# Kernel tuning notes

Measured on AMD Instinct MI355X. Metric: run time of the kernel, lower is better.

The kernel has to match this reference:

```python
import jax, jax.numpy as jnp
import numpy as np

N_NODES = 50000
N_EDGES = 800000
IN_CH = 128
HID = 32
HEADS = 4
OUT_CH = 16
NEG_SLOPE = 0.2  # PyG GATConv default LeakyReLU slope


def setup_inputs() -> dict:
    key = jax.random.key(0)
    ks = jax.random.split(key, 12)
    x = jax.random.normal(ks[0], (N_NODES, IN_CH), dtype=jnp.float32)
    edge_index = jax.random.randint(ks[1], (2, N_EDGES), 0, N_NODES, dtype=jnp.int32)
    edge_attr = jax.random.uniform(ks[2], (N_EDGES,), dtype=jnp.float32)
    s = 0.1
    W1 = jax.random.normal(ks[3], (IN_CH, HEADS * HID), dtype=jnp.float32) * s
    a_src1 = jax.random.normal(ks[4], (HEADS, HID), dtype=jnp.float32) * s
    a_dst1 = jax.random.normal(ks[5], (HEADS, HID), dtype=jnp.float32) * s
    b1 = jnp.zeros((HEADS * HID,), dtype=jnp.float32)
    W2 = jax.random.normal(ks[6], (HEADS * HID, OUT_CH), dtype=jnp.float32) * s
    a_src2 = jax.random.normal(ks[7], (1, OUT_CH), dtype=jnp.float32) * s
    a_dst2 = jax.random.normal(ks[8], (1, OUT_CH), dtype=jnp.float32) * s
    b2 = jnp.zeros((OUT_CH,), dtype=jnp.float32)
    return {"x": x, "edge_index": edge_index, "edge_attr": edge_attr,
            "W1": W1, "a_src1": a_src1, "a_dst1": a_dst1, "b1": b1,
            "W2": W2, "a_src2": a_src2, "a_dst2": a_dst2, "b2": b2}


def gat_conv(x, src, dst, num_nodes, W, a_src, a_dst, bias, concat):
    H, C = a_src.shape
    h = (x @ W).reshape(-1, H, C)              # [N,H,C]
    al_src = jnp.sum(h * a_src, axis=-1)       # [N,H]
    al_dst = jnp.sum(h * a_dst, axis=-1)       # [N,H]
    e = jax.nn.leaky_relu(al_src[src] + al_dst[dst], NEG_SLOPE)  # [E,H]
    # segment softmax over incoming edges of each destination node
    m = jax.ops.segment_max(e, dst, num_segments=num_nodes)
    ex = jnp.exp(e - m[dst])
    denom = jax.ops.segment_sum(ex, dst, num_segments=num_nodes)
    alpha = ex / (denom[dst] + 1e-16)          # [E,H]
    out = jax.ops.segment_sum(h[src] * alpha[..., None], dst, num_segments=num_nodes)  # [N,H,C]
    out = out.reshape(num_nodes, H * C) if concat else out.mean(axis=1)
    return out + bias


def reference(x, edge_index, edge_attr, W1, a_src1, a_dst1, b1, W2, a_src2, a_dst2, b2):
    # edge_attr is ignored by GATConv when edge_dim is None (PyG default)
    N = x.shape[0]
    loop = jnp.arange(N, dtype=edge_index.dtype)  # PyG add_self_loops=True
    src = jnp.concatenate([edge_index[0], loop])
    dst = jnp.concatenate([edge_index[1], loop])
    h = jax.nn.elu(gat_conv(x, src, dst, N, W1, a_src1, a_dst1, b1, True))
    out = gat_conv(h, src, dst, N, W2, a_src2, a_dst2, b2, False)
    return jax.nn.log_softmax(out, axis=1)
```

## Files before the change

### kernel.cpp

```cpp
#include <hip/hip_runtime.h>

#define N_NODESC 50000
#define E0C      800000
#define E_TOTC   850000
#define IN_CHC   128
#define HCC      128
#define HEADSC   4
#define OUT_CHC  16
#define NEG_SLOPE 0.2f
#define G1_ROWS  32
#define NBUCK    196
#define BNODES   256
#define SBLK     128
#define CHUNK    6656

__device__ __forceinline__ float lrelu(float v){ return v > 0.f ? v : NEG_SLOPE * v; }

__device__ __forceinline__ unsigned int f2bf(float f){
  unsigned int b = __float_as_uint(f);
  return (b + 0x7fffu + ((b >> 16) & 1u)) >> 16;
}
__device__ __forceinline__ float bf2f(unsigned int lo16){
  return __uint_as_float(lo16 << 16);
}
__device__ __forceinline__ int xswz(int r, int k){ return r ^ (((k >> 4) & 7) << 2); }

__global__ void __launch_bounds__(512) k_gemm1(const float* __restrict__ x, const float* __restrict__ W1,
        const float* __restrict__ a_s, const float* __restrict__ a_d,
        unsigned int* __restrict__ h1b, float* __restrict__ al_s, float* __restrict__ al_d)
{
  __shared__ __align__(16) float Wl[IN_CHC*HCC];
  __shared__ __align__(16) float xT[IN_CHC][G1_ROWS];
  int tid = threadIdx.x;
  for (int i = tid*4; i < IN_CHC*HCC; i += 512*4)
    *(float4*)&Wl[i] = *(const float4*)&W1[i];
  int row0 = blockIdx.x * G1_ROWS;
  {
    int r  = tid >> 4;
    int kc = (tid & 15) * 8;
    int rr = row0 + r; if (rr > N_NODESC-1) rr = N_NODESC-1;
    const float* xp = &x[(size_t)rr*IN_CHC + kc];
    int sc = xswz(r, kc);
    #pragma unroll
    for (int j = 0; j < 8; j += 4){
      float4 v = *(const float4*)&xp[j];
      xT[kc+j+0][sc] = v.x;
      xT[kc+j+1][sc] = v.y;
      xT[kc+j+2][sc] = v.z;
      xT[kc+j+3][sc] = v.w;
    }
  }
  __syncthreads();
  int wave = tid >> 6, lane = tid & 63;
  int c0 = lane * 2;
  int rbase = wave * 4;
  float acc[4][2];
  #pragma unroll
  for (int j = 0; j < 4; j++){ acc[j][0] = 0.f; acc[j][1] = 0.f; }
  #pragma unroll 4
  for (int k = 0; k < IN_CHC; k++){
    float2 w  = *(const float2*)&Wl[k*HCC + c0];
    float4 xa = *(const float4*)&xT[k][xswz(rbase, k)];
    acc[0][0] = fmaf(xa.x, w.x, acc[0][0]); acc[0][1] = fmaf(xa.x, w.y, acc[0][1]);
    acc[1][0] = fmaf(xa.y, w.x, acc[1][0]); acc[1][1] = fmaf(xa.y, w.y, acc[1][1]);
    acc[2][0] = fmaf(xa.z, w.x, acc[2][0]); acc[2][1] = fmaf(xa.z, w.y, acc[2][1]);
    acc[3][0] = fmaf(xa.w, w.x, acc[3][0]); acc[3][1] = fmaf(xa.w, w.y, acc[3][1]);
  }
  float as0 = a_s[c0], as1 = a_s[c0+1];
  float ad0 = a_d[c0], ad1 = a_d[c0+1];
  #pragma unroll
  for (int j = 0; j < 4; j++){
    int row = row0 + rbase + j;
    if (row >= N_NODESC) break;
    h1b[(size_t)row*64 + lane] = f2bf(acc[j][0]) | (f2bf(acc[j][1]) << 16);
    float ps = acc[j][0]*as0 + acc[j][1]*as1;
    float pd = acc[j][0]*ad0 + acc[j][1]*ad1;
    #pragma unroll
    for (int m = 1; m < 16; m <<= 1){ ps += __shfl_xor(ps, m, 64); pd += __shfl_xor(pd, m, 64); }
    if ((lane & 15) == 0){
      al_s[row*HEADSC + (lane>>4)] = ps;
      al_d[row*HEADSC + (lane>>4)] = pd;
    }
  }
}

__global__ void __launch_bounds__(256) k_binA(const int* __restrict__ ei, int* __restrict__ bh){
  __shared__ int h[NBUCK];
  int tid = threadIdx.x, b = blockIdx.x;
  for (int i = tid; i < NBUCK; i += 256) h[i] = 0;
  __syncthreads();
  int e0 = b*CHUNK, e1 = e0 + CHUNK; if (e1 > E_TOTC) e1 = E_TOTC;
  for (int e = e0 + tid; e < e1; e += 256){
    int d = (e < E0C) ? ei[E0C + e] : (e - E0C);
    atomicAdd(&h[d >> 8], 1);
  }
  __syncthreads();
  for (int i = tid; i < NBUCK; i += 256) bh[b*NBUCK + i] = h[i];
}

__global__ void __launch_bounds__(256) k_binscan(int* __restrict__ bh, int* __restrict__ bstart){
  __shared__ int buf[256];
  int tid = threadIdx.x;
  int tot = 0;
  if (tid < NBUCK)
    for (int b = 0; b < SBLK; b++) tot += bh[b*NBUCK + tid];
  buf[tid] = (tid < NBUCK) ? tot : 0;
  __syncthreads();
  #pragma unroll
  for (int off = 1; off < 256; off <<= 1){
    int t = (tid >= off) ? buf[tid - off] : 0;
    __syncthreads();
    buf[tid] += t; __syncthreads();
  }
  int excl = buf[tid] - ((tid < NBUCK) ? tot : 0);
  if (tid < NBUCK) bstart[tid] = excl;
  if (tid == 0) bstart[NBUCK] = E_TOTC;
  __syncthreads();
  if (tid < NBUCK){
    int run = excl;
    for (int b = 0; b < SBLK; b++){
      int t = bh[b*NBUCK + tid];
      bh[b*NBUCK + tid] = run;
      run += t;
    }
  }
}

__global__ void __launch_bounds__(256) k_binB(const int* __restrict__ ei, const int* __restrict__ bh,
                                              unsigned int* __restrict__ binbuf){
  __shared__ int h[NBUCK];
  int tid = threadIdx.x, b = blockIdx.x;
  for (int i = tid; i < NBUCK; i += 256) h[i] = bh[b*NBUCK + i];
  __syncthreads();
  int e0 = b*CHUNK, e1 = e0 + CHUNK; if (e1 > E_TOTC) e1 = E_TOTC;
  for (int e = e0 + tid; e < e1; e += 256){
    int s, d;
    if (e < E0C){ d = ei[E0C + e]; s = ei[e]; }
    else { s = e - E0C; d = s; }
    int pos = atomicAdd(&h[d >> 8], 1);
    binbuf[pos] = ((unsigned int)d << 16) | (unsigned int)s;
  }
}

__global__ void __launch_bounds__(256) k_binC(const unsigned int* __restrict__ binbuf,
                                              const int* __restrict__ bstart,
                                              int* __restrict__ rp, int* __restrict__ srcs){
  __shared__ int lcnt[BNODES];
  __shared__ int buf[BNODES];
  __shared__ int pfx[BNODES];
  int tid = threadIdx.x, k = blockIdx.x;
  int lo = k * BNODES;
  int b0 = bstart[k], b1 = bstart[k+1];
  lcnt[tid] = 0;
  __syncthreads();
  for (int i = b0 + tid; i < b1; i += 256){
    int d = binbuf[i] >> 16;
    atomicAdd(&lcnt[d - lo], 1);
  }
  __syncthreads();
  int v = lcnt[tid];
  buf[tid] = v;
  __syncthreads();
  #pragma unroll
  for (int off = 1; off < 256; off <<= 1){
    int t = (tid >= off) ? buf[tid - off] : 0;
    __syncthreads();
    buf[tid] += t; __syncthreads();
  }
  int excl = buf[tid] - v;
  pfx[tid] = excl;
  int node = lo + tid;
  if (node < N_NODESC) rp[node] = b0 + excl;
  if (k == 0 && tid == 0) rp[N_NODESC] = E_TOTC;
  lcnt[tid] = 0;
  __syncthreads();
  for (int i = b0 + tid; i < b1; i += 256){
    unsigned int u = binbuf[i];
    int d = u >> 16;
    int r = atomicAdd(&lcnt[d - lo], 1);
    srcs[b0 + pfx[d - lo] + r] = (int)(u & 0xffffu);
  }
}

__global__ void __launch_bounds__(256) k_node1(const unsigned int* __restrict__ h1b,
        const float* __restrict__ al_s, const float* __restrict__ al_d,
        const int* __restrict__ rp, const int* __restrict__ srcs,
        const float* __restrict__ b1, float* __restrict__ hout)
{
  int wave = threadIdx.x >> 6, lane = threadIdx.x & 63;
  int n = blockIdx.x*4 + wave;
  if (n >= N_NODESC) return;
  int beg = rp[n], end = rp[n+1];
  int h = lane >> 4;
  float adh = al_d[n*4 + h];
  float dsum = 0.f, acc0 = 0.f, acc1 = 0.f;
  #pragma unroll 4
  for (int p = beg; p < end; p++){
    int s = srcs[p];
    float a = __expf(lrelu(al_s[s*4 + h] + adh));
    unsigned int u = h1b[(size_t)s*64 + lane];
    dsum += a;
    acc0 = fmaf(a, bf2f(u & 0xffffu), acc0);
    acc1 = fmaf(a, bf2f(u >> 16), acc1);
  }
  float inv = 1.f / (dsum + 1e-16f);
  int c0 = lane*2;
  float o0 = acc0*inv + b1[c0], o1 = acc1*inv + b1[c0+1];
  o0 = o0 > 0.f ? o0 : __expf(o0) - 1.f;
  o1 = o1 > 0.f ? o1 : __expf(o1) - 1.f;
  *(float2*)&hout[(size_t)n*HCC + c0] = make_float2(o0, o1);
}

__global__ void __launch_bounds__(256) k_gemm2(const float* __restrict__ hin, const float* __restrict__ W2,
        const float* __restrict__ a_s, const float* __restrict__ a_d,
        float* __restrict__ h2, float* __restrict__ al_s, float* __restrict__ al_d)
{
  __shared__ __align__(16) float Wl[IN_CHC*OUT_CHC];
  __shared__ __align__(16) float xr[4][4][IN_CHC];
  int tid = threadIdx.x;
  for (int i = tid*4; i < IN_CHC*OUT_CHC; i += 256*4)
    *(float4*)&Wl[i] = *(const float4*)&W2[i];
  __syncthreads();
  int wave = tid >> 6, lane = tid & 63;
  int r = lane >> 4, c = lane & 15;
  int row0 = blockIdx.x*16 + wave*4;
  for (int rr = 0; rr < 4; rr++){
    float2 v = *(const float2*)&hin[(size_t)(row0+rr)*IN_CHC + lane*2];
    *(float2*)&xr[wave][rr][lane*2] = v;
  }
  float acc = 0.f;
  #pragma unroll 8
  for (int k = 0; k < IN_CHC; k++)
    acc = fmaf(xr[wave][r][k], Wl[k*OUT_CHC + c], acc);
  int row = row0 + r;
  h2[row*OUT_CHC + c] = acc;
  float ps = acc * a_s[c];
  float pd = acc * a_d[c];
  #pragma unroll
  for (int m = 1; m < 16; m <<= 1){ ps += __shfl_xor(ps, m, 64); pd += __shfl_xor(pd, m, 64); }
  if (c == 0){ al_s[row] = ps; al_d[row] = pd; }
}

__global__ void __launch_bounds__(256) k_node2(const float* __restrict__ h2,
        const float* __restrict__ al_s, const float* __restrict__ al_d,
        const int* __restrict__ rp, const int* __restrict__ srcs,
        const float* __restrict__ b2, float* __restrict__ out)
{
  int wave = threadIdx.x >> 6, lane = threadIdx.x & 63;
  int n = blockIdx.x*4 + wave;
  if (n >= N_NODESC) return;
  int beg = rp[n], end = rp[n+1];
  float ad = al_d[n];
  int c = lane & 15, jg = lane >> 4;
  float dsum = 0.f, acc = 0.f;
  #pragma unroll 4
  for (int p = beg + jg; p < end; p += 4){
    int s = srcs[p];
    float a = __expf(lrelu(al_s[s] + ad));
    dsum += a;
    acc = fmaf(a, h2[s*OUT_CHC + c], acc);
  }
  dsum += __shfl_xor(dsum, 16, 64);
  dsum += __shfl_xor(dsum, 32, 64);
  acc += __shfl_xor(acc, 16, 64);
  acc += __shfl_xor(acc, 32, 64);
  float inv = 1.f / (dsum + 1e-16f);
  float v = acc*inv + b2[c];
  float mm = v;
  #pragma unroll
  for (int o = 1; o < 16; o <<= 1) mm = fmaxf(mm, __shfl_xor(mm, o, 64));
  float se = __expf(v - mm);
  #pragma unroll
  for (int o = 1; o < 16; o <<= 1) se += __shfl_xor(se, o, 64);
  if (jg == 0) out[n*OUT_CHC + c] = v - mm - __logf(se);
}

extern "C" void kernel_launch(void* const* d_in, const int* in_sizes, int n_in,
                              void* d_out, int out_size, void* d_ws, size_t ws_size,
                              hipStream_t stream)
{
  const float* x   = (const float*)d_in[0];
  const int*   ei  = (const int*)d_in[1];
  const float* W1  = (const float*)d_in[3];
  const float* as1 = (const float*)d_in[4];
  const float* ad1 = (const float*)d_in[5];
  const float* b1  = (const float*)d_in[6];
  const float* W2  = (const float*)d_in[7];
  const float* as2 = (const float*)d_in[8];
  const float* ad2 = (const float*)d_in[9];
  const float* b2  = (const float*)d_in[10];
  float* out = (float*)d_out;

  char* ws = (char*)d_ws;
  size_t off = 0;
  auto alloc = [&](size_t bytes)->void*{
    void* p = ws + off;
    off = (off + bytes + 255) & ~(size_t)255;
    return p;
  };
  unsigned int* h1b = (unsigned int*)alloc((size_t)N_NODESC*64*4);
  float* hout  = (float*)alloc((size_t)N_NODESC*HCC*4);
  float* al_s1 = (float*)alloc((size_t)N_NODESC*HEADSC*4);
  float* al_d1 = (float*)alloc((size_t)N_NODESC*HEADSC*4);
  float* h2    = (float*)alloc((size_t)N_NODESC*OUT_CHC*4);
  float* al_s2 = (float*)alloc((size_t)N_NODESC*4);
  float* al_d2 = (float*)alloc((size_t)N_NODESC*4);
  int* rp      = (int*)alloc((size_t)(N_NODESC+1)*4);
  int* srcs    = (int*)alloc((size_t)E_TOTC*4);
  int* bh      = (int*)alloc((size_t)SBLK*NBUCK*4);
  int* bstart  = (int*)alloc((size_t)(NBUCK+1)*4);
  unsigned int* binbuf = (unsigned int*)alloc((size_t)E_TOTC*4);

  k_gemm1<<<(N_NODESC+G1_ROWS-1)/G1_ROWS, 512, 0, stream>>>(x, W1, as1, ad1, h1b, al_s1, al_d1);
  k_binA<<<SBLK, 256, 0, stream>>>(ei, bh);
  k_binscan<<<1, 256, 0, stream>>>(bh, bstart);
  k_binB<<<SBLK, 256, 0, stream>>>(ei, bh, binbuf);
  k_binC<<<NBUCK, 256, 0, stream>>>(binbuf, bstart, rp, srcs);
  k_node1<<<(N_NODESC+3)/4, 256, 0, stream>>>(h1b, al_s1, al_d1, rp, srcs, b1, hout);
  k_gemm2<<<N_NODESC/16, 256, 0, stream>>>(hout, W2, as2, ad2, h2, al_s2, al_d2);
  k_node2<<<(N_NODESC+3)/4, 256, 0, stream>>>(h2, al_s2, al_d2, rp, srcs, b2, out);
}
```

Baseline: 168.9 us.

## Store W1 in LDS and layer-2 features h2 as packed bf16

Converts W1 to packed bf16 when loading it into shared memory in the first GEMM, which halves its LDS footprint (64KB to 32KB) and may allow more blocks per CU. It also stores the layer-2 node features h2 as packed bf16 pairs, halving the bytes gathered per edge in the second aggregation kernel. Both reduce precision: W1 is rounded before the FMA, and h2 loses mantissa bits, which could push results past the tolerance.

```diff
diff --git a/kernel.cpp b/kernel.cpp
--- a/kernel.cpp
+++ b/kernel.cpp
@@ -29,11 +29,13 @@
         const float* __restrict__ a_s, const float* __restrict__ a_d,
         unsigned int* __restrict__ h1b, float* __restrict__ al_s, float* __restrict__ al_d)
 {
-  __shared__ __align__(16) float Wl[IN_CHC*HCC];
+  __shared__ __align__(16) unsigned int Wl[IN_CHC*HCC/2];
   __shared__ __align__(16) float xT[IN_CHC][G1_ROWS];
   int tid = threadIdx.x;
-  for (int i = tid*4; i < IN_CHC*HCC; i += 512*4)
-    *(float4*)&Wl[i] = *(const float4*)&W1[i];
+  for (int i = tid; i < IN_CHC*HCC/2; i += 512){
+    float2 w = *(const float2*)&W1[(size_t)i*2];
+    Wl[i] = f2bf(w.x) | (f2bf(w.y) << 16);
+  }
   int row0 = blockIdx.x * G1_ROWS;
   {
     int r  = tid >> 4;
@@ -59,12 +61,14 @@
   for (int j = 0; j < 4; j++){ acc[j][0] = 0.f; acc[j][1] = 0.f; }
   #pragma unroll 4
   for (int k = 0; k < IN_CHC; k++){
-    float2 w  = *(const float2*)&Wl[k*HCC + c0];
+    unsigned int uw = Wl[k*64 + lane];
+    float wx = __uint_as_float(uw << 16);
+    float wy = __uint_as_float(uw & 0xFFFF0000u);
     float4 xa = *(const float4*)&xT[k][xswz(rbase, k)];
-    acc[0][0] = fmaf(xa.x, w.x, acc[0][0]); acc[0][1] = fmaf(xa.x, w.y, acc[0][1]);
-    acc[1][0] = fmaf(xa.y, w.x, acc[1][0]); acc[1][1] = fmaf(xa.y, w.y, acc[1][1]);
-    acc[2][0] = fmaf(xa.z, w.x, acc[2][0]); acc[2][1] = fmaf(xa.z, w.y, acc[2][1]);
-    acc[3][0] = fmaf(xa.w, w.x, acc[3][0]); acc[3][1] = fmaf(xa.w, w.y, acc[3][1]);
+    acc[0][0] = fmaf(xa.x, wx, acc[0][0]); acc[0][1] = fmaf(xa.x, wy, acc[0][1]);
+    acc[1][0] = fmaf(xa.y, wx, acc[1][0]); acc[1][1] = fmaf(xa.y, wy, acc[1][1]);
+    acc[2][0] = fmaf(xa.z, wx, acc[2][0]); acc[2][1] = fmaf(xa.z, wy, acc[2][1]);
+    acc[3][0] = fmaf(xa.w, wx, acc[3][0]); acc[3][1] = fmaf(xa.w, wy, acc[3][1]);
   }
   float as0 = a_s[c0], as1 = a_s[c0+1];
   float ad0 = a_d[c0], ad1 = a_d[c0+1];
@@ -213,7 +217,7 @@
 
 __global__ void __launch_bounds__(256) k_gemm2(const float* __restrict__ hin, const float* __restrict__ W2,
         const float* __restrict__ a_s, const float* __restrict__ a_d,
-        float* __restrict__ h2, float* __restrict__ al_s, float* __restrict__ al_d)
+        unsigned int* __restrict__ h2b, float* __restrict__ al_s, float* __restrict__ al_d)
 {
   __shared__ __align__(16) float Wl[IN_CHC*OUT_CHC];
   __shared__ __align__(16) float xr[4][4][IN_CHC];
@@ -233,7 +237,9 @@
   for (int k = 0; k < IN_CHC; k++)
     acc = fmaf(xr[wave][r][k], Wl[k*OUT_CHC + c], acc);
   int row = row0 + r;
-  h2[row*OUT_CHC + c] = acc;
+  float other = __shfl_xor(acc, 1, 64);
+  if ((c & 1) == 0)
+    h2b[(size_t)row*8 + (c >> 1)] = f2bf(acc) | (f2bf(other) << 16);
   float ps = acc * a_s[c];
   float pd = acc * a_d[c];
   #pragma unroll
@@ -241,7 +247,7 @@
   if (c == 0){ al_s[row] = ps; al_d[row] = pd; }
 }
 
-__global__ void __launch_bounds__(256) k_node2(const float* __restrict__ h2,
+__global__ void __launch_bounds__(256) k_node2(const unsigned int* __restrict__ h2b,
         const float* __restrict__ al_s, const float* __restrict__ al_d,
         const int* __restrict__ rp, const int* __restrict__ srcs,
         const float* __restrict__ b2, float* __restrict__ out)
@@ -252,13 +258,17 @@
   int beg = rp[n], end = rp[n+1];
   float ad = al_d[n];
   int c = lane & 15, jg = lane >> 4;
+  unsigned int hi = (c & 1);
+  int widx = c >> 1;
   float dsum = 0.f, acc = 0.f;
   #pragma unroll 4
   for (int p = beg + jg; p < end; p += 4){
     int s = srcs[p];
     float a = __expf(lrelu(al_s[s] + ad));
+    unsigned int u = h2b[(size_t)s*8 + widx];
+    float hv = __uint_as_float(hi ? (u & 0xFFFF0000u) : (u << 16));
     dsum += a;
-    acc = fmaf(a, h2[s*OUT_CHC + c], acc);
+    acc = fmaf(a, hv, acc);
   }
   dsum += __shfl_xor(dsum, 16, 64);
   dsum += __shfl_xor(dsum, 32, 64);
@@ -302,7 +312,7 @@
   float* hout  = (float*)alloc((size_t)N_NODESC*HCC*4);
   float* al_s1 = (float*)alloc((size_t)N_NODESC*HEADSC*4);
   float* al_d1 = (float*)alloc((size_t)N_NODESC*HEADSC*4);
-  float* h2    = (float*)alloc((size_t)N_NODESC*OUT_CHC*4);
+  unsigned int* h2b = (unsigned int*)alloc((size_t)N_NODESC*8*4);
   float* al_s2 = (float*)alloc((size_t)N_NODESC*4);
   float* al_d2 = (float*)alloc((size_t)N_NODESC*4);
   int* rp      = (int*)alloc((size_t)(N_NODESC+1)*4);
@@ -317,6 +327,6 @@
   k_binB<<<SBLK, 256, 0, stream>>>(ei, bh, binbuf);
   k_binC<<<NBUCK, 256, 0, stream>>>(binbuf, bstart, rp, srcs);
   k_node1<<<(N_NODESC+3)/4, 256, 0, stream>>>(h1b, al_s1, al_d1, rp, srcs, b1, hout);
-  k_gemm2<<<N_NODESC/16, 256, 0, stream>>>(hout, W2, as2, ad2, h2, al_s2, al_d2);
-  k_node2<<<(N_NODESC+3)/4, 256, 0, stream>>>(h2, al_s2, al_d2, rp, srcs, b2, out);
-}
+  k_gemm2<<<N_NODESC/16, 256, 0, stream>>>(hout, W2, as2, ad2, h2b, al_s2, al_d2);
+  k_node2<<<(N_NODESC+3)/4, 256, 0, stream>>>(h2b, al_s2, al_d2, rp, srcs, b2, out);
+}
```

Measured after the change: 165.6 us. About the same (-1.9%).
